# Optimization experiments

Measured on AMD Instinct MI355X. Metric: run time of the kernel, lower is better.

The kernel has to match this reference:

```python
import jax, jax.numpy as jnp
import numpy as np

D_MODEL, D_STATE, D_CONV = 768, 8, 3
D_INNER = D_MODEL  # expand = 1
BATCH, SEQ = 4, 8192


def setup_inputs() -> dict:
    key = jax.random.key(0)
    ks = jax.random.split(key, 7)
    x = jax.random.normal(ks[0], (BATCH, SEQ, D_MODEL), dtype=jnp.float32)
    W_in = jax.random.normal(ks[1], (D_MODEL, 2 * D_INNER), dtype=jnp.float32) * 0.02
    conv_w = jax.random.normal(ks[2], (D_INNER, 1, D_CONV), dtype=jnp.float32) * 0.1
    conv_b = jnp.zeros((D_INNER,), dtype=jnp.float32)
    B = jax.random.normal(ks[3], (D_INNER, D_STATE), dtype=jnp.float32)
    C = jax.random.normal(ks[4], (D_INNER, D_STATE), dtype=jnp.float32)
    D = jnp.ones((D_INNER,), dtype=jnp.float32)
    W_out = jax.random.normal(ks[5], (D_INNER, D_MODEL), dtype=jnp.float32) * 0.02
    return {"x": x, "W_in": W_in, "conv_w": conv_w, "conv_b": conv_b,
            "B": B, "C": C, "D": D, "W_out": W_out}


def _forward(x, W_in, conv_w, conv_b, B, C, D, W_out):
    # in_proj and chunk
    xz = x @ W_in                                   # [B, L, 2*d_inner]
    xc, z = jnp.split(xz, 2, axis=-1)               # each [B, L, d_inner]
    # depthwise causal conv1d: torch pads (d_conv-1) both sides then slices [:L]
    # == left-pad (d_conv-1), no right pad
    xc = jnp.transpose(xc, (0, 2, 1))               # [B, d_inner, L]
    xc = jax.lax.conv_general_dilated(
        xc, conv_w,
        window_strides=(1,), padding=[(D_CONV - 1, 0)],
        dimension_numbers=("NCH", "OIH", "NCH"),
        feature_group_count=D_INNER)
    xc = xc + conv_b[None, :, None]
    xc = jnp.transpose(xc, (0, 2, 1))               # [B, L, d_inner]
    xc = jax.nn.silu(xc)
    z = jax.nn.silu(z)
    # simple SSM: h_t = h_{t-1} + outer(u_t, B); y_t = sum_s h_t*C + u_t*D
    # => y = cumsum_t(u) * sum_s(B*C) + u*D   (exact algebraic identity)
    BC = jnp.sum(B * C, axis=-1)                    # [d_inner]
    y = jnp.cumsum(xc, axis=1) * BC + xc * D
    out = (y * z) @ W_out                           # [B, L, d_model]
    return out


def reference(x, W_in, conv_w, conv_b, B, C, D, W_out):
    return _forward(x, W_in, conv_w, conv_b, B, C, D, W_out)
```

## Files before the change

### kernel.cpp

```cpp
#include <hip/hip_runtime.h>
#include <hip/hip_bf16.h>

#define D_MODEL 768
#define NSEQ    8192
#define NBATCH  4
#define MROWS   (NBATCH*NSEQ)
#define CHUNK   128
#define NCHUNK  (NSEQ/CHUNK)

#define BM 128
#define BN 192
#define BK 64

typedef __attribute__((ext_vector_type(8)))  short bshort8;
typedef __attribute__((ext_vector_type(16))) float f32x16;

__device__ __forceinline__ float bf2f(ushort u){
  union { unsigned int i; float f; } x; x.i = ((unsigned int)u) << 16; return x.f;
}
__device__ __forceinline__ ushort f2bf(float f){
  union { float f; unsigned int i; } x; x.f = f;
  unsigned int r = x.i + 0x7fffu + ((x.i >> 16) & 1u);
  return (ushort)(r >> 16);
}
__device__ __forceinline__ float silu_f(float v){ return v / (1.0f + __expf(-v)); }

__device__ __forceinline__ void async_copy16(const ushort* g, ushort* l){
  __builtin_amdgcn_global_load_lds((const __attribute__((address_space(1))) void*)g,
                                   (__attribute__((address_space(3))) void*)l, 16, 0, 0);
}

__global__ void tr_cvt(const float* __restrict__ in, ushort* __restrict__ out, int R, int C){
  __shared__ float tile[32][33];
  int c0 = blockIdx.x*32, r0 = blockIdx.y*32;
  int tx = threadIdx.x & 31, ty = threadIdx.x >> 5;
  #pragma unroll
  for (int p=0;p<4;p++){
    int r = ty + p*8;
    tile[r][tx] = in[(size_t)(r0+r)*C + c0 + tx];
  }
  __syncthreads();
  #pragma unroll
  for (int p=0;p<4;p++){
    int c = ty + p*8;
    out[(size_t)(c0+c)*R + r0 + tx] = f2bf(tile[tx][c]);
  }
}

__global__ void cvt_bf16(const float* __restrict__ in, ushort* __restrict__ out, int n){
  int i = (blockIdx.x*256 + threadIdx.x)*8;
  if (i >= n) return;
  const float4 f0 = *(const float4*)(in + i);
  const float4 f1 = *(const float4*)(in + i + 4);
  ushort o[8];
  o[0]=f2bf(f0.x); o[1]=f2bf(f0.y); o[2]=f2bf(f0.z); o[3]=f2bf(f0.w);
  o[4]=f2bf(f1.x); o[5]=f2bf(f1.y); o[6]=f2bf(f1.z); o[7]=f2bf(f1.w);
  *(ulonglong2*)(out + i) = *(const ulonglong2*)o;
}

__global__ __launch_bounds__(256) void gemm1_bt(
    const ushort* __restrict__ A, const ushort* __restrict__ BT,
    ushort* __restrict__ oxc, ushort* __restrict__ oz, int K)
{
  __shared__ __align__(16) ushort Asm[BM*BK];
  __shared__ __align__(16) ushort Bsm[BN*BK];
  const int tid = threadIdx.x;
  const int bm = blockIdx.x, bn = blockIdx.y;
  const int lane = tid & 63, wid = tid >> 6;
  const int wm = (wid >> 1) * 64, wn = (wid & 1) * 96;
  const int l31 = lane & 31, half = lane >> 5;

  const ushort* Ag[4]; ushort* Al[4];
  #pragma unroll
  for (int it=0; it<4; ++it){
    int p  = it*256 + tid;
    int r  = p >> 3;
    int cl = (p & 7) ^ (r & 7);
    Ag[it] = A + (size_t)(bm*BM + r)*K + cl*8;
    Al[it] = Asm + p*8;
  }
  const ushort* Bg[6]; ushort* Bl[6];
  #pragma unroll
  for (int it=0; it<6; ++it){
    int p  = it*256 + tid;
    int r  = p >> 3;
    int cl = (p & 7) ^ (r & 7);
    Bg[it] = BT + (size_t)(bn*BN + r)*K + cl*8;
    Bl[it] = Bsm + p*8;
  }

  int arow[2], ar7[2], brow[3], br7[3];
  #pragma unroll
  for (int i=0;i<2;i++){
    int ra = wm + i*32 + l31; arow[i] = ra*BK; ar7[i] = ra & 7;
  }
  #pragma unroll
  for (int j=0;j<3;j++){
    int rb = wn + j*32 + l31; brow[j] = rb*BK; br7[j] = rb & 7;
  }

  f32x16 acc[2][3];
  #pragma unroll
  for (int i=0;i<2;i++)
    #pragma unroll
    for (int j=0;j<3;j++)
      #pragma unroll
      for (int r=0;r<16;r++) acc[i][j][r] = 0.f;

  const int KT = K / BK;
  for (int kt=0; kt<KT; ++kt){
    __syncthreads();
    #pragma unroll
    for (int it=0; it<4; ++it){ async_copy16(Ag[it], Al[it]); Ag[it] += BK; }
    #pragma unroll
    for (int it=0; it<6; ++it){ async_copy16(Bg[it], Bl[it]); Bg[it] += BK; }
    asm volatile("s_waitcnt vmcnt(0)" ::: "memory");
    __syncthreads();

    #pragma unroll
    for (int s=0; s<4; ++s){
      const int c = s*2 + half;
      bshort8 av[2], bv[3];
      #pragma unroll
      for (int i=0;i<2;i++)
        av[i] = *(const bshort8*)(Asm + arow[i] + ((c ^ ar7[i]) << 3));
      #pragma unroll
      for (int j=0;j<3;j++)
        bv[j] = *(const bshort8*)(Bsm + brow[j] + ((c ^ br7[j]) << 3));
      #pragma unroll
      for (int i=0;i<2;i++)
        #pragma unroll
        for (int j=0;j<3;j++)
          acc[i][j] = __builtin_amdgcn_mfma_f32_32x32x16_bf16(av[i], bv[j], acc[i][j], 0,0,0);
    }
  }

  if (bn < 4){
    #pragma unroll
    for (int i=0;i<2;i++){
      const int Rbase = bm*BM + wm + i*32 + 4*half;
      #pragma unroll
      for (int j=0;j<3;j++){
        const int Cc = bn*BN + wn + j*32 + l31;
        #pragma unroll
        for (int reg=0; reg<16; reg++){
          const int R = Rbase + (reg & 3) + 8*(reg >> 2);
          oxc[(size_t)R*768 + Cc] = f2bf(acc[i][j][reg]);
        }
      }
    }
  } else {
    #pragma unroll
    for (int i=0;i<2;i++){
      const int Rbase = bm*BM + wm + i*32 + 4*half;
      #pragma unroll
      for (int j=0;j<3;j++){
        const int Cc = bn*BN - 768 + wn + j*32 + l31;
        #pragma unroll
        for (int reg=0; reg<16; reg++){
          const int R = Rbase + (reg & 3) + 8*(reg >> 2);
          oz[(size_t)R*768 + Cc] = f2bf(silu_f(acc[i][j][reg]));
        }
      }
    }
  }
}

#define BM2 64
__global__ __launch_bounds__(256) void gemm2_bt(
    const ushort* __restrict__ A, const ushort* __restrict__ BT,
    float* __restrict__ of, int K)
{
  __shared__ __align__(16) ushort Asm[BM2*BK];
  __shared__ __align__(16) ushort Bsm[BN*BK];
  const int tid = threadIdx.x;
  const int bm = blockIdx.x, bn = blockIdx.y;
  const int lane = tid & 63, wid = tid >> 6;
  const int wm = (wid >> 1) * 32, wn = (wid & 1) * 96;
  const int l31 = lane & 31, half = lane >> 5;

  const ushort* Ag[2]; ushort* Al[2];
  #pragma unroll
  for (int it=0; it<2; ++it){
    int p  = it*256 + tid;
    int r  = p >> 3;
    int cl = (p & 7) ^ (r & 7);
    Ag[it] = A + (size_t)(bm*BM2 + r)*K + cl*8;
    Al[it] = Asm + p*8;
  }
  const ushort* Bg[6]; ushort* Bl[6];
  #pragma unroll
  for (int it=0; it<6; ++it){
    int p  = it*256 + tid;
    int r  = p >> 3;
    int cl = (p & 7) ^ (r & 7);
    Bg[it] = BT + (size_t)(bn*BN + r)*K + cl*8;
    Bl[it] = Bsm + p*8;
  }

  int arow, ar7, brow[3], br7[3];
  { int ra = wm + l31; arow = ra*BK; ar7 = ra & 7; }
  #pragma unroll
  for (int j=0;j<3;j++){
    int rb = wn + j*32 + l31; brow[j] = rb*BK; br7[j] = rb & 7;
  }

  f32x16 acc[3];
  #pragma unroll
  for (int j=0;j<3;j++)
    #pragma unroll
    for (int r=0;r<16;r++) acc[j][r] = 0.f;

  const int KT = K / BK;
  for (int kt=0; kt<KT; ++kt){
    __syncthreads();
    #pragma unroll
    for (int it=0; it<2; ++it){ async_copy16(Ag[it], Al[it]); Ag[it] += BK; }
    #pragma unroll
    for (int it=0; it<6; ++it){ async_copy16(Bg[it], Bl[it]); Bg[it] += BK; }
    asm volatile("s_waitcnt vmcnt(0)" ::: "memory");
    __syncthreads();

    #pragma unroll
    for (int s=0; s<4; ++s){
      const int c = s*2 + half;
      bshort8 av, bv[3];
      av = *(const bshort8*)(Asm + arow + ((c ^ ar7) << 3));
      #pragma unroll
      for (int j=0;j<3;j++)
        bv[j] = *(const bshort8*)(Bsm + brow[j] + ((c ^ br7[j]) << 3));
      #pragma unroll
      for (int j=0;j<3;j++)
        acc[j] = __builtin_amdgcn_mfma_f32_32x32x16_bf16(av, bv[j], acc[j], 0,0,0);
    }
  }

  const int Rbase = bm*BM2 + wm + 4*half;
  #pragma unroll
  for (int j=0;j<3;j++){
    const int Cc = bn*BN + wn + j*32 + l31;
    #pragma unroll
    for (int reg=0; reg<16; reg++){
      const int R = Rbase + (reg & 3) + 8*(reg >> 2);
      of[(size_t)R*768 + Cc] = acc[j][reg];
    }
  }
}

__global__ void conv_psum(const ushort* __restrict__ xc, const float* __restrict__ cw,
                          const float* __restrict__ cb, float* __restrict__ psum){
  int c0 = threadIdx.x * 2;
  int b = blockIdx.z, ch = blockIdx.x;
  int t0 = ch*CHUNK;
  const ushort* xp = xc + (size_t)b*NSEQ*768 + c0;
  float w0a=cw[c0*3+0], w1a=cw[c0*3+1], w2a=cw[c0*3+2], ba=cb[c0];
  float w0b=cw[c0*3+3], w1b=cw[c0*3+4], w2b=cw[c0*3+5], bb=cb[c0+1];
  float am2=0.f, am1=0.f, bm2=0.f, bm1=0.f;
  if (t0>=2){ ushort2 u = *(const ushort2*)(xp + (size_t)(t0-2)*768); am2=bf2f(u.x); bm2=bf2f(u.y); }
  if (t0>=1){ ushort2 u = *(const ushort2*)(xp + (size_t)(t0-1)*768); am1=bf2f(u.x); bm1=bf2f(u.y); }
  float sa=0.f, sb=0.f;
  #pragma unroll 4
  for (int i=0;i<CHUNK;i++){
    ushort2 u = *(const ushort2*)(xp + (size_t)(t0+i)*768);
    float xa = bf2f(u.x), xb = bf2f(u.y);
    sa += silu_f(w0a*am2 + w1a*am1 + w2a*xa + ba);
    sb += silu_f(w0b*bm2 + w1b*bm1 + w2b*xb + bb);
    am2=am1; am1=xa; bm2=bm1; bm1=xb;
  }
  float2* pp = (float2*)(psum + ((size_t)b*NCHUNK + ch)*768 + c0);
  *pp = make_float2(sa, sb);
}

__global__ void scan_chunks(const float* __restrict__ psum, float* __restrict__ offs){
  int idx = blockIdx.x*256 + threadIdx.x;
  int b = idx/768, c = idx%768;
  float run = 0.f;
  for (int ch=0; ch<NCHUNK; ch++){
    size_t o = ((size_t)b*NCHUNK + ch)*768 + c;
    offs[o] = run;
    run += psum[o];
  }
}

__global__ void scan_apply(const ushort* __restrict__ xc, const ushort* __restrict__ zb,
                           const float* __restrict__ cw, const float* __restrict__ cb,
                           const float* __restrict__ Bm, const float* __restrict__ Cm,
                           const float* __restrict__ Dv, const float* __restrict__ offs,
                           ushort* __restrict__ v){
  int c0 = threadIdx.x * 2;
  int b = blockIdx.z, ch = blockIdx.x;
  int t0 = ch*CHUNK;
  size_t base = (size_t)b*NSEQ*768 + c0;
  const ushort* xp = xc + base;
  const ushort* zp = zb + base;
  ushort* vp = v + base;
  float w0a=cw[c0*3+0], w1a=cw[c0*3+1], w2a=cw[c0*3+2], ba=cb[c0];
  float w0b=cw[c0*3+3], w1b=cw[c0*3+4], w2b=cw[c0*3+5], bb=cb[c0+1];
  float bca=0.f, bcb=0.f;
  #pragma unroll
  for (int s=0;s<8;s++){ bca += Bm[c0*8+s]*Cm[c0*8+s]; bcb += Bm[c0*8+8+s]*Cm[c0*8+8+s]; }
  float dda = Dv[c0], ddb = Dv[c0+1];
  const float2 off2 = *(const float2*)(offs + ((size_t)b*NCHUNK + ch)*768 + c0);
  float cua = off2.x, cub = off2.y;
  float am2=0.f, am1=0.f, bm2=0.f, bm1=0.f;
  if (t0>=2){ ushort2 u = *(const ushort2*)(xp + (size_t)(t0-2)*768); am2=bf2f(u.x); bm2=bf2f(u.y); }
  if (t0>=1){ ushort2 u = *(const ushort2*)(xp + (size_t)(t0-1)*768); am1=bf2f(u.x); bm1=bf2f(u.y); }
  #pragma unroll 4
  for (int i=0;i<CHUNK;i++){
    size_t o = (size_t)(t0+i)*768;
    ushort2 u = *(const ushort2*)(xp + o);
    ushort2 z2 = *(const ushort2*)(zp + o);
    float xa = bf2f(u.x), xb = bf2f(u.y);
    float ua = silu_f(w0a*am2 + w1a*am1 + w2a*xa + ba);
    float ub = silu_f(w0b*bm2 + w1b*bm1 + w2b*xb + bb);
    cua += ua; cub += ub;
    float ya = bca*cua + dda*ua;
    float yb = bcb*cub + ddb*ub;
    ushort2 o2; o2.x = f2bf(ya * bf2f(z2.x)); o2.y = f2bf(yb * bf2f(z2.y));
    *(ushort2*)(vp + o) = o2;
    am2=am1; am1=xa; bm2=bm1; bm1=xb;
  }
}

extern "C" void kernel_launch(void* const* d_in, const int* in_sizes, int n_in,
                              void* d_out, int out_size, void* d_ws, size_t ws_size,
                              hipStream_t stream)
{
  const float* x      = (const float*)d_in[0];
  const float* W_in   = (const float*)d_in[1];
  const float* conv_w = (const float*)d_in[2];
  const float* conv_b = (const float*)d_in[3];
  const float* Bm     = (const float*)d_in[4];
  const float* Cm     = (const float*)d_in[5];
  const float* Dv     = (const float*)d_in[6];
  const float* W_out  = (const float*)d_in[7];
  float* out = (float*)d_out;

  char* ws = (char*)d_ws;
  ushort* xbf   = (ushort*)(ws + 0);
  ushort* xcbf  = (ushort*)(ws + 50331648);
  ushort* zbf   = (ushort*)(ws + 100663296);
  ushort* wint  = (ushort*)(ws + 150994944);
  ushort* woutt = (ushort*)(ws + 153354240);
  float*  psum  = (float*)(ws + 154533888);
  float*  offs  = (float*)(ws + 155320320);
  if (ws_size < 156106752) return;

  tr_cvt<<<dim3(1536/32, 768/32), 256, 0, stream>>>(W_in,  wint,  768, 1536);
  tr_cvt<<<dim3(768/32,  768/32), 256, 0, stream>>>(W_out, woutt, 768, 768);
  cvt_bf16<<<(MROWS*768)/2048, 256, 0, stream>>>(x, xbf, MROWS*768);

  gemm1_bt<<<dim3(MROWS/BM, 1536/BN), 256, 0, stream>>>(xbf, wint, xcbf, zbf, 768);

  conv_psum  <<<dim3(NCHUNK, 1, NBATCH), 384, 0, stream>>>(xcbf, conv_w, conv_b, psum);
  scan_chunks<<<12, 256, 0, stream>>>(psum, offs);
  scan_apply <<<dim3(NCHUNK, 1, NBATCH), 384, 0, stream>>>(xcbf, zbf, conv_w, conv_b,
                                                           Bm, Cm, Dv, offs, xbf );

  gemm2_bt<<<dim3(MROWS/BM2, 768/BN), 256, 0, stream>>>(xbf, woutt, out, 768);
}
```

Baseline: 407.7 us.

## Fuse fp32-to-bf16 input conversion into GEMM1 and parallelize chunk scan with wave shuffles

Removes the separate x-to-bf16 conversion kernel by having gemm1 load fp32 rows directly, convert them in registers and store bf16 into shared memory. This saves a full read/write pass over the activations and a workspace buffer. Chunk size is halved to raise parallelism in the conv/scan kernels. The chunk-offset scan becomes one wave per (batch, channel), using shuffle-based prefix sums instead of a serial loop over 12 blocks. scan_apply now writes its output in place over the z buffer. The catch is that gemm1 A loads become synchronous global loads, which are no longer async copies, and they double the bytes fetched per tile.

```diff
diff --git a/kernel.cpp b/kernel.cpp
--- a/kernel.cpp
+++ b/kernel.cpp
@@ -5,7 +5,7 @@
 #define NSEQ    8192
 #define NBATCH  4
 #define MROWS   (NBATCH*NSEQ)
-#define CHUNK   128
+#define CHUNK   64
 #define NCHUNK  (NSEQ/CHUNK)
 
 #define BM 128
@@ -47,21 +47,11 @@
   }
 }
 
-__global__ void cvt_bf16(const float* __restrict__ in, ushort* __restrict__ out, int n){
-  int i = (blockIdx.x*256 + threadIdx.x)*8;
-  if (i >= n) return;
-  const float4 f0 = *(const float4*)(in + i);
-  const float4 f1 = *(const float4*)(in + i + 4);
-  ushort o[8];
-  o[0]=f2bf(f0.x); o[1]=f2bf(f0.y); o[2]=f2bf(f0.z); o[3]=f2bf(f0.w);
-  o[4]=f2bf(f1.x); o[5]=f2bf(f1.y); o[6]=f2bf(f1.z); o[7]=f2bf(f1.w);
-  *(ulonglong2*)(out + i) = *(const ulonglong2*)o;
-}
-
 __global__ __launch_bounds__(256) void gemm1_bt(
-    const ushort* __restrict__ A, const ushort* __restrict__ BT,
-    ushort* __restrict__ oxc, ushort* __restrict__ oz, int K)
+    const float* __restrict__ Af, const ushort* __restrict__ BT,
+    ushort* __restrict__ oxc, ushort* __restrict__ oz)
 {
+  const int K = 768;
   __shared__ __align__(16) ushort Asm[BM*BK];
   __shared__ __align__(16) ushort Bsm[BN*BK];
   const int tid = threadIdx.x;
@@ -70,14 +60,14 @@
   const int wm = (wid >> 1) * 64, wn = (wid & 1) * 96;
   const int l31 = lane & 31, half = lane >> 5;
 
-  const ushort* Ag[4]; ushort* Al[4];
+  const float* Ag[4]; int Ap[4];
   #pragma unroll
   for (int it=0; it<4; ++it){
     int p  = it*256 + tid;
     int r  = p >> 3;
     int cl = (p & 7) ^ (r & 7);
-    Ag[it] = A + (size_t)(bm*BM + r)*K + cl*8;
-    Al[it] = Asm + p*8;
+    Ag[it] = Af + (size_t)(bm*BM + r)*K + cl*8;
+    Ap[it] = p*8;
   }
   const ushort* Bg[6]; ushort* Bl[6];
   #pragma unroll
@@ -111,9 +101,23 @@
   for (int kt=0; kt<KT; ++kt){
     __syncthreads();
     #pragma unroll
-    for (int it=0; it<4; ++it){ async_copy16(Ag[it], Al[it]); Ag[it] += BK; }
-    #pragma unroll
     for (int it=0; it<6; ++it){ async_copy16(Bg[it], Bl[it]); Bg[it] += BK; }
+    float4 f0[4], f1[4];
+    #pragma unroll
+    for (int it=0; it<4; ++it){
+      f0[it] = *(const float4*)(Ag[it]);
+      f1[it] = *(const float4*)(Ag[it] + 4);
+      Ag[it] += BK;
+    }
+    #pragma unroll
+    for (int it=0; it<4; ++it){
+      __hip_bfloat162 h[4];
+      h[0] = __float22bfloat162_rn(make_float2(f0[it].x, f0[it].y));
+      h[1] = __float22bfloat162_rn(make_float2(f0[it].z, f0[it].w));
+      h[2] = __float22bfloat162_rn(make_float2(f1[it].x, f1[it].y));
+      h[3] = __float22bfloat162_rn(make_float2(f1[it].z, f1[it].w));
+      *(ulonglong2*)(Asm + Ap[it]) = *(const ulonglong2*)h;
+    }
     asm volatile("s_waitcnt vmcnt(0)" ::: "memory");
     __syncthreads();
 
@@ -272,21 +276,30 @@
 }
 
 __global__ void scan_chunks(const float* __restrict__ psum, float* __restrict__ offs){
-  int idx = blockIdx.x*256 + threadIdx.x;
-  int b = idx/768, c = idx%768;
-  float run = 0.f;
-  for (int ch=0; ch<NCHUNK; ch++){
-    size_t o = ((size_t)b*NCHUNK + ch)*768 + c;
-    offs[o] = run;
-    run += psum[o];
-  }
-}
-
-__global__ void scan_apply(const ushort* __restrict__ xc, const ushort* __restrict__ zb,
+  int wv   = (blockIdx.x*256 + threadIdx.x) >> 6;
+  int lane = threadIdx.x & 63;
+  int b = wv / 768, c = wv % 768;
+  size_t base = ((size_t)b*NCHUNK)*768 + c;
+  int ch0 = lane*2;
+  float v0 = psum[base + (size_t)ch0*768];
+  float v1 = psum[base + (size_t)(ch0+1)*768];
+  float pair = v0 + v1;
+  float inc = pair;
+  #pragma unroll
+  for (int d=1; d<64; d<<=1){
+    float t = __shfl_up(inc, d, 64);
+    if (lane >= d) inc += t;
+  }
+  float excl = inc - pair;
+  offs[base + (size_t)ch0*768]     = excl;
+  offs[base + (size_t)(ch0+1)*768] = excl + v0;
+}
+
+__global__ void scan_apply(const ushort* __restrict__ xc, const ushort* zb,
                            const float* __restrict__ cw, const float* __restrict__ cb,
                            const float* __restrict__ Bm, const float* __restrict__ Cm,
                            const float* __restrict__ Dv, const float* __restrict__ offs,
-                           ushort* __restrict__ v){
+                           ushort* v){
   int c0 = threadIdx.x * 2;
   int b = blockIdx.z, ch = blockIdx.x;
   int t0 = ch*CHUNK;
@@ -337,25 +350,23 @@
   float* out = (float*)d_out;
 
   char* ws = (char*)d_ws;
-  ushort* xbf   = (ushort*)(ws + 0);
-  ushort* xcbf  = (ushort*)(ws + 50331648);
-  ushort* zbf   = (ushort*)(ws + 100663296);
-  ushort* wint  = (ushort*)(ws + 150994944);
-  ushort* woutt = (ushort*)(ws + 153354240);
-  float*  psum  = (float*)(ws + 154533888);
-  float*  offs  = (float*)(ws + 155320320);
-  if (ws_size < 156106752) return;
+  ushort* xcbf  = (ushort*)(ws + 0);
+  ushort* zbf   = (ushort*)(ws + 50331648);
+  ushort* wint  = (ushort*)(ws + 100663296);
+  ushort* woutt = (ushort*)(ws + 103022592);
+  float*  psum  = (float*)(ws + 104202240);
+  float*  offs  = (float*)(ws + 105775104);
+  if (ws_size < 107347968) return;
 
   tr_cvt<<<dim3(1536/32, 768/32), 256, 0, stream>>>(W_in,  wint,  768, 1536);
   tr_cvt<<<dim3(768/32,  768/32), 256, 0, stream>>>(W_out, woutt, 768, 768);
-  cvt_bf16<<<(MROWS*768)/2048, 256, 0, stream>>>(x, xbf, MROWS*768);
-
-  gemm1_bt<<<dim3(MROWS/BM, 1536/BN), 256, 0, stream>>>(xbf, wint, xcbf, zbf, 768);
+
+  gemm1_bt<<<dim3(MROWS/BM, 1536/BN), 256, 0, stream>>>(x, wint, xcbf, zbf);
 
   conv_psum  <<<dim3(NCHUNK, 1, NBATCH), 384, 0, stream>>>(xcbf, conv_w, conv_b, psum);
-  scan_chunks<<<12, 256, 0, stream>>>(psum, offs);
+  scan_chunks<<<768, 256, 0, stream>>>(psum, offs);
   scan_apply <<<dim3(NCHUNK, 1, NBATCH), 384, 0, stream>>>(xcbf, zbf, conv_w, conv_b,
-                                                           Bm, Cm, Dv, offs, xbf );
-
-  gemm2_bt<<<dim3(MROWS/BM2, 768/BN), 256, 0, stream>>>(xbf, woutt, out, 768);
-}
+                                                           Bm, Cm, Dv, offs, zbf );
+
+  gemm2_bt<<<dim3(MROWS/BM2, 768/BN), 256, 0, stream>>>(zbf, woutt, out, 768);
+}
```

Result: slower. 508.7 us (+24.8%).
